# Kernel tuning notes

Measured on AMD Instinct MI355X. Metric: run time of the kernel, lower is better.

Reference implementation:

```python
import jax, jax.numpy as jnp
import numpy as np
from jax import lax

N_LAYERS = 4
D_MODEL = 256
D_INNER = 512   # expand * d_model
D_STATE = 16
D_CONV = 4
DT_RANK = 16    # ceil(d_model/16)
N_FEATURES = 32
N_CLASSES = 3
BATCH, SEQ = 8, 2048


def _layernorm(x, w, b, eps=1e-5):
    mu = x.mean(-1, keepdims=True)
    var = ((x - mu) ** 2).mean(-1, keepdims=True)
    return (x - mu) * lax.rsqrt(var + eps) * w + b


def _silu(x):
    return x * jax.nn.sigmoid(x)


def _ssm(xc, xpW, dtW, dtB, A_log, D):
    # xc: (B,S,d_inner)
    xd = xc @ xpW                                    # (B,S,dt_rank+2*d_state)
    dt_r = xd[..., :DT_RANK]
    Bm = xd[..., DT_RANK:DT_RANK + D_STATE]          # (B,S,N)
    Cm = xd[..., DT_RANK + D_STATE:]                 # (B,S,N)
    dt = jax.nn.softplus(dt_r @ dtW + dtB)           # (B,S,d_inner)
    A = -jnp.exp(A_log)                              # (d_inner,N)
    dA = jnp.exp(dt[..., None] * A)                  # (B,S,d_inner,N)
    dBx = dt[..., None] * Bm[:, :, None, :] * xc[..., None]  # (B,S,d_inner,N)

    def step(h, inp):
        dA_t, dBx_t, C_t = inp                       # (B,d_inner,N),(B,d_inner,N),(B,N)
        h = dA_t * h + dBx_t
        y_t = (h * C_t[:, None, :]).sum(-1)          # (B,d_inner)
        return h, y_t

    h0 = jnp.zeros((xc.shape[0], D_INNER, D_STATE), xc.dtype)
    xs = (dA.transpose(1, 0, 2, 3), dBx.transpose(1, 0, 2, 3), Cm.transpose(1, 0, 2))
    _, ys = lax.scan(step, h0, xs)                   # (S,B,d_inner)
    y = ys.transpose(1, 0, 2)
    return y + xc * D


def _mamba_block(x, inW, convW, convB, xpW, dtW, dtB, A_log, D, outW):
    xz = x @ inW                                     # (B,S,2*d_inner)
    xs, z = xz[..., :D_INNER], xz[..., D_INNER:]
    # causal depthwise conv1d (left-pad d_conv-1)
    xp = jnp.pad(xs, ((0, 0), (D_CONV - 1, 0), (0, 0)))
    xc = lax.conv_general_dilated(
        xp, convW, window_strides=(1,), padding='VALID',
        dimension_numbers=('NWC', 'WIO', 'NWC'),
        feature_group_count=D_INNER) + convB
    xc = _silu(xc)
    y = _ssm(xc, xpW, dtW, dtB, A_log, D)
    y = y * _silu(z)
    return y @ outW


def setup_inputs() -> dict:
    key = jax.random.key(0)
    ks = jax.random.split(key, 20)
    s = 0.02
    L = N_LAYERS
    inp = {
        'x': jax.random.normal(ks[0], (BATCH, SEQ, N_FEATURES), jnp.float32),
        'in_w': jax.random.normal(ks[1], (N_FEATURES, D_MODEL), jnp.float32) * s,
        'in_b': jnp.zeros((D_MODEL,), jnp.float32),
        'ln_w': jnp.ones((L, D_MODEL), jnp.float32),
        'ln_b': jnp.zeros((L, D_MODEL), jnp.float32),
        'inW': jax.random.normal(ks[2], (L, D_MODEL, 2 * D_INNER), jnp.float32) * s,
        'convW': jax.random.normal(ks[3], (L, D_CONV, 1, D_INNER), jnp.float32) * s,
        'convB': jnp.zeros((L, D_INNER), jnp.float32),
        'xpW': jax.random.normal(ks[4], (L, D_INNER, DT_RANK + 2 * D_STATE), jnp.float32) * s,
        'dtW': jax.random.uniform(ks[5], (L, DT_RANK, D_INNER), jnp.float32,
                                  -DT_RANK ** -0.5, DT_RANK ** -0.5),
        'A_log': jnp.broadcast_to(jnp.log(jnp.arange(1, D_STATE + 1, dtype=jnp.float32)),
                                  (L, D_INNER, D_STATE)).copy(),
        'D': jnp.ones((L, D_INNER), jnp.float32),
        'outW': jax.random.normal(ks[6], (L, D_INNER, D_MODEL), jnp.float32) * s,
        'fln_w': jnp.ones((D_MODEL,), jnp.float32),
        'fln_b': jnp.zeros((D_MODEL,), jnp.float32),
        'h1W': jax.random.normal(ks[7], (D_MODEL, D_MODEL // 2), jnp.float32) * s,
        'h1b': jnp.zeros((D_MODEL // 2,), jnp.float32),
        'h2W': jax.random.normal(ks[8], (D_MODEL // 2, N_CLASSES), jnp.float32) * s,
        'h2b': jnp.zeros((N_CLASSES,), jnp.float32),
    }
    # dt bias init: inv softplus of dt ~ LogUniform(dt_min, dt_max)
    dt_min, dt_max = 1e-3, 0.1
    u = jax.random.uniform(ks[9], (L, D_INNER), jnp.float32)
    dt = jnp.clip(jnp.exp(u * (np.log(dt_max) - np.log(dt_min)) + np.log(dt_min)), 1e-4)
    inp['dtB'] = dt + jnp.log(-jnp.expm1(-dt))
    return inp


def reference(x, in_w, in_b, ln_w, ln_b, inW, convW, convB, xpW, dtW, dtB,
              A_log, D, outW, fln_w, fln_b, h1W, h1b, h2W, h2b):
    h = x @ in_w + in_b                              # (B,S,d_model); dropout is eval-mode identity
    for i in range(N_LAYERS):
        h = h + _mamba_block(_layernorm(h, ln_w[i], ln_b[i]),
                             inW[i], convW[i], convB[i], xpW[i],
                             dtW[i], dtB[i], A_log[i], D[i], outW[i])
    h = _layernorm(h, fln_w, fln_b)
    last = h[:, -1]                                  # (B,d_model)
    hidden = jax.nn.gelu(last @ h1W + h1b)
    return hidden @ h2W + h2b                        # (B,n_classes)
```

## Files before the change

### kernel.cpp

```cpp
#include <hip/hip_runtime.h>
#include <math.h>

namespace {

constexpr int NL = 4;
constexpr int DM = 256;
constexpr int DI = 512;
constexpr int DS = 16;
constexpr int DR = 16;
constexpr int NF = 32;
constexpr int NB = 8;
constexpr int T  = 2048;
constexpr int ROWS = NB * T;
constexpr int XD = DR + 2 * DS;
constexpr int NC = 64;
constexpr int CL = T / NC;
constexpr int SCN = NB * DI * DS;

constexpr float LOG2E = 1.44269504088896341f;
constexpr float LN2   = 0.69314718055994531f;

typedef __attribute__((ext_vector_type(4))) float f32x4;
typedef __attribute__((ext_vector_type(8))) short bf16x8;
typedef __attribute__((ext_vector_type(4))) short s16x4;

__device__ __forceinline__ float fexp2(float x) { return __builtin_amdgcn_exp2f(x); }
__device__ __forceinline__ float frcp(float x)  { return __builtin_amdgcn_rcpf(x); }
__device__ __forceinline__ float flog2(float x) { return __builtin_amdgcn_logf(x); }

__device__ __forceinline__ float siluf(float x) {
    return x * frcp(1.f + fexp2(-LOG2E * x));
}
__device__ __forceinline__ float softplusf(float x) {
    return fmaxf(x, 0.f) + LN2 * flog2(1.f + fexp2(-LOG2E * fabsf(x)));
}
__device__ __forceinline__ short f2bf(float f) {
    union { float f; unsigned u; } c; c.f = f;
    unsigned r = (c.u + 0x7FFFu + ((c.u >> 16) & 1u)) >> 16;
    return (short)r;
}
__device__ __forceinline__ float bf2f(short s) {
    union { unsigned u; float f; } c; c.u = ((unsigned)(unsigned short)s) << 16;
    return c.f;
}
__device__ __forceinline__ void powers16(float g, float* a) {
    float g2 = g * g, g4 = g2 * g2, g8 = g4 * g4;
    a[0] = g;        a[1] = g2;       a[2] = g * g2;   a[3] = g4;
    a[4] = g * g4;   a[5] = g2 * g4;  a[6] = a[2] * g4; a[7] = g8;
    a[8] = g * g8;   a[9] = g2 * g8;  a[10] = a[2] * g8; a[11] = g4 * g8;
    a[12] = a[4] * g8; a[13] = a[5] * g8; a[14] = a[6] * g8; a[15] = g8 * g8;
}

__global__ void wtrans(const float* __restrict__ src, short* __restrict__ dst,
                       int K, int N, int Npad, int perL_dst)
{
    const int idx = blockIdx.x * 256 + threadIdx.x;
    const int l = idx / perL_dst;
    const int r = idx - l * perL_dst;
    const unsigned n = (unsigned)r / (unsigned)K;
    const unsigned k = (unsigned)r - n * (unsigned)K;
    float v = (n < (unsigned)N) ? src[(size_t)l * K * N + k * N + n] : 0.f;
    dst[idx] = f2bf(v);
}

__global__ void prep_dtWt(const float* __restrict__ dtW, float* __restrict__ dtWt)
{
    const int idx = blockIdx.x * 256 + threadIdx.x;
    const int l = idx / (DI * DR);
    const int r0 = idx - l * (DI * DR);
    const int d = r0 / DR, rr = r0 - d * DR;
    dtWt[idx] = dtW[(size_t)l * DR * DI + rr * DI + d];
}

__global__ void prep_A2(const float* __restrict__ A_log, float* __restrict__ negA2)
{
    const int i = blockIdx.x * 256 + threadIdx.x;
    negA2[i] = -LOG2E * fexp2(LOG2E * A_log[i]);
}

__global__ void cvt_bf16(const float* __restrict__ src, short* __restrict__ dst)
{
    const int i = blockIdx.x * 256 + threadIdx.x;
    dst[i] = f2bf(src[i]);
}

template <int EP>
__global__ void gemm_mfma(const short* __restrict__ A, const short* __restrict__ Bt,
                          float* __restrict__ C, short* __restrict__ Cs0,
                          short* __restrict__ Cs1, const float* __restrict__ bias,
                          int K, int lda, int ldc, int Ncut, int NXB, int NYB)
{
    __shared__ short smem[7680];
    const int bid = blockIdx.x;
    const int xcd = bid & 7, j = bid >> 3;
    const int by = xcd * (NYB >> 3) + j / NXB;
    const int bx = j - (j / NXB) * NXB;
    const int m0 = by * 128;
    const int n0 = bx * 64;

    const int tid = threadIdx.x;
    const int lane = tid & 63, w = tid >> 6;
    const int wr = w >> 1, wc = w & 1;
    const int lr = lane & 15, lk = lane >> 4;

    f32x4 acc[4][2] = {};
    for (int k0 = 0; k0 < K; k0 += 32) {
        __syncthreads();
#pragma unroll
        for (int i = 0; i < 2; ++i) {
            int c = tid + i * 256;
            int row = c >> 2, seg = c & 3;
            bf16x8 v = *(const bf16x8*)(A + (size_t)(m0 + row) * lda + k0 + seg * 8);
            *(bf16x8*)(&smem[row * 40 + seg * 8]) = v;
        }
        {
            int row = tid >> 2, seg = tid & 3;
            bf16x8 v = *(const bf16x8*)(Bt + (size_t)(n0 + row) * K + k0 + seg * 8);
            *(bf16x8*)(&smem[5120 + row * 40 + seg * 8]) = v;
        }
        __syncthreads();
        bf16x8 af[4], bfr[2];
#pragma unroll
        for (int m = 0; m < 4; ++m)
            af[m] = *(const bf16x8*)(&smem[(wr * 64 + m * 16 + lr) * 40 + lk * 8]);
#pragma unroll
        for (int n = 0; n < 2; ++n)
            bfr[n] = *(const bf16x8*)(&smem[5120 + (wc * 32 + n * 16 + lr) * 40 + lk * 8]);
#pragma unroll
        for (int m = 0; m < 4; ++m)
#pragma unroll
            for (int n = 0; n < 2; ++n)
                acc[m][n] = __builtin_amdgcn_mfma_f32_16x16x32_bf16(af[m], bfr[n], acc[m][n], 0, 0, 0);
    }
#pragma unroll
    for (int m = 0; m < 4; ++m) {
#pragma unroll
        for (int n = 0; n < 2; ++n) {
            const int col = n0 + wc * 32 + n * 16 + lr;
#pragma unroll
            for (int j2 = 0; j2 < 4; ++j2) {
                const int row = m0 + wr * 64 + m * 16 + lk * 4 + j2;
                const float v = acc[m][n][j2];
                if (EP == 0) {
                    if (col < DI) Cs0[(size_t)row * DI + col] = f2bf(v);
                    else          Cs1[(size_t)row * DI + col - DI] = f2bf(siluf(v));
                } else if (EP == 1) {
                    if (col < Ncut) C[(size_t)row * ldc + col] = v;
                } else if (EP == 2) {
                    C[(size_t)row * ldc + col] += v;
                } else {
                    C[(size_t)row * ldc + col] = v + bias[col];
                }
            }
        }
    }
}

__global__ void layernorm_kernel(const float* __restrict__ x,
                                 const float* __restrict__ w,
                                 const float* __restrict__ b,
                                 short* __restrict__ out)
{
    const int row = blockIdx.x;
    const int t = threadIdx.x;
    const int wid = t >> 6, lane = t & 63;
    __shared__ float red[4];

    float v = x[row * DM + t];
    float s = v;
#pragma unroll
    for (int o = 32; o >= 1; o >>= 1) s += __shfl_xor(s, o);
    if (lane == 0) red[wid] = s;
    __syncthreads();
    float mu = (red[0] + red[1] + red[2] + red[3]) * (1.f / DM);
    __syncthreads();

    float d = v - mu;
    float q = d * d;
#pragma unroll
    for (int o = 32; o >= 1; o >>= 1) q += __shfl_xor(q, o);
    if (lane == 0) red[wid] = q;
    __syncthreads();
    float var = (red[0] + red[1] + red[2] + red[3]) * (1.f / DM);

    out[row * DM + t] = f2bf(d * (1.f / sqrtf(var + 1e-5f)) * w[t] + b[t]);
}

__global__ void conv_silu_kernel(const short* __restrict__ xsb,
                                 const float* __restrict__ W,
                                 const float* __restrict__ Bc,
                                 short* __restrict__ xcb)
{
    const int idx = blockIdx.x * 256 + threadIdx.x;
    const int c4 = idx & (DI / 4 - 1);
    const int bt = idx >> 7;
    const int t = bt & (T - 1);
    const int c = c4 * 4;
    f32x4 acc = *(const f32x4*)(Bc + c);
#pragma unroll
    for (int k = 0; k < 4; ++k) {
        int tt = t + k - 3;
        if (tt >= 0) {
            s16x4 v = *(const s16x4*)(xsb + (size_t)(bt + k - 3) * DI + c);
            f32x4 wv = *(const f32x4*)(W + k * DI + c);
#pragma unroll
            for (int q = 0; q < 4; ++q) acc[q] += bf2f(v[q]) * wv[q];
        }
    }
    s16x4 o;
#pragma unroll
    for (int q = 0; q < 4; ++q) o[q] = f2bf(siluf(acc[q]));
    *(s16x4*)(xcb + (size_t)idx * 4) = o;
}

__global__ void scan_pass1(const float* __restrict__ xd,
                           const short* __restrict__ xcb,
                           const float* __restrict__ negA2,
                           const float* __restrict__ dtWt,
                           const float* __restrict__ dtB,
                           float* __restrict__ P, float* __restrict__ S)
{
    __shared__ float lds[CL][32];
    const int d = blockIdx.x * 256 + threadIdx.x;
    const int c = blockIdx.y;
    const int b = blockIdx.z;
    const int row0 = b * T + c * CL;

    {
        int t = threadIdx.x >> 3, seg = threadIdx.x & 7;
        *(f32x4*)&lds[t][seg * 4] =
            *(const f32x4*)(xd + (size_t)(row0 + t) * XD + seg * 4);
    }
    float A2[DS], h[DS], wcol[DR];
#pragma unroll
    for (int q = 0; q < 4; ++q) {
        *(f32x4*)&A2[q * 4]   = *(const f32x4*)(negA2 + d * DS + q * 4);
        *(f32x4*)&wcol[q * 4] = *(const f32x4*)(dtWt + d * DR + q * 4);
    }
    bool fastb = true;
#pragma unroll
    for (int s = 1; s < DS; ++s)
        fastb = fastb && (fabsf(A2[s] - A2[0] * (float)(s + 1)) <= 1e-4f * fabsf(A2[s]));
    const bool fast = __all(fastb);
#pragma unroll
    for (int s = 0; s < DS; ++s) h[s] = 0.f;
    const float dtBd = dtB[d];
    float sdt = 0.f;
    __syncthreads();

    for (int t = 0; t < CL; ++t) {
        float xcv = bf2f(xcb[(size_t)(row0 + t) * DI + d]);
        float accd = dtBd;
#pragma unroll
        for (int q = 0; q < 4; ++q) {
            f32x4 xr = *(const f32x4*)&lds[t][q * 4];
            accd += xr[0] * wcol[q * 4] + xr[1] * wcol[q * 4 + 1]
                  + xr[2] * wcol[q * 4 + 2] + xr[3] * wcol[q * 4 + 3];
        }
        float dtv = softplusf(accd);
        float dx = dtv * xcv;
        sdt += dtv;
        float a[DS];
        if (fast) powers16(fexp2(dtv * A2[0]), a);
        else {
#pragma unroll
            for (int s = 0; s < DS; ++s) a[s] = fexp2(dtv * A2[s]);
        }
#pragma unroll
        for (int q = 0; q < 4; ++q) {
            f32x4 Bv = *(const f32x4*)&lds[t][16 + q * 4];
#pragma unroll
            for (int s = 0; s < 4; ++s)
                h[q * 4 + s] = a[q * 4 + s] * h[q * 4 + s] + dx * Bv[s];
        }
    }
    float pa[DS];
    if (fast) powers16(fexp2(A2[0] * sdt), pa);
    else {
#pragma unroll
        for (int s = 0; s < DS; ++s) pa[s] = fexp2(A2[s] * sdt);
    }
    const size_t base = (size_t)c * SCN + ((size_t)b * DI + d) * DS;
#pragma unroll
    for (int q = 0; q < 4; ++q) {
        *(f32x4*)(S + base + q * 4) = *(f32x4*)&h[q * 4];
        *(f32x4*)(P + base + q * 4) = *(f32x4*)&pa[q * 4];
    }
}

__global__ void scan_combine(float* __restrict__ P, const float* __restrict__ S)
{
    const int idx3 = blockIdx.x * blockDim.x + threadIdx.x;
    float h = 0.f;
    for (int c = 0; c < NC; ++c) {
        float pc = P[c * SCN + idx3];
        float sc = S[c * SCN + idx3];
        P[c * SCN + idx3] = h;
        h = pc * h + sc;
    }
}

__global__ void scan_pass2(const float* __restrict__ xd,
                           const short* __restrict__ xcb,
                           const float* __restrict__ negA2,
                           const float* __restrict__ dtWt,
                           const float* __restrict__ dtB,
                           const float* __restrict__ Dv,
                           const float* __restrict__ H,
                           const short* __restrict__ zgb,
                           short* __restrict__ yb)
{
    __shared__ float lds[CL][48];
    const int d = blockIdx.x * 256 + threadIdx.x;
    const int c = blockIdx.y;
    const int b = blockIdx.z;
    const int row0 = b * T + c * CL;

    for (int c0 = threadIdx.x; c0 < CL * 12; c0 += 256) {
        int t = c0 / 12, seg = c0 - t * 12;
        *(f32x4*)&lds[t][seg * 4] =
            *(const f32x4*)(xd + (size_t)(row0 + t) * XD + seg * 4);
    }
    float A2[DS], h[DS], wcol[DR];
#pragma unroll
    for (int q = 0; q < 4; ++q) {
        *(f32x4*)&A2[q * 4]   = *(const f32x4*)(negA2 + d * DS + q * 4);
        *(f32x4*)&wcol[q * 4] = *(const f32x4*)(dtWt + d * DR + q * 4);
    }
    bool fastb = true;
#pragma unroll
    for (int s = 1; s < DS; ++s)
        fastb = fastb && (fabsf(A2[s] - A2[0] * (float)(s + 1)) <= 1e-4f * fabsf(A2[s]));
    const bool fast = __all(fastb);
    const size_t base = (size_t)c * SCN + ((size_t)b * DI + d) * DS;
#pragma unroll
    for (int q = 0; q < 4; ++q)
        *(f32x4*)&h[q * 4] = *(const f32x4*)(H + base + q * 4);
    const float dtBd = dtB[d];
    const float Dd = Dv[d];
    __syncthreads();

    for (int t = 0; t < CL; ++t) {
        const size_t row = (size_t)(row0 + t);
        float xcv = bf2f(xcb[row * DI + d]);
        float zg  = bf2f(zgb[row * DI + d]);
        float accd = dtBd;
#pragma unroll
        for (int q = 0; q < 4; ++q) {
            f32x4 xr = *(const f32x4*)&lds[t][q * 4];
            accd += xr[0] * wcol[q * 4] + xr[1] * wcol[q * 4 + 1]
                  + xr[2] * wcol[q * 4 + 2] + xr[3] * wcol[q * 4 + 3];
        }
        float dtv = softplusf(accd);
        float dx = dtv * xcv;
        float a[DS];
        if (fast) powers16(fexp2(dtv * A2[0]), a);
        else {
#pragma unroll
            for (int s = 0; s < DS; ++s) a[s] = fexp2(dtv * A2[s]);
        }
        float acc0 = 0.f, acc1 = 0.f, acc2 = 0.f, acc3 = 0.f;
#pragma unroll
        for (int q = 0; q < 4; ++q) {
            f32x4 Bv = *(const f32x4*)&lds[t][16 + q * 4];
            f32x4 Cv = *(const f32x4*)&lds[t][32 + q * 4];
            h[q * 4 + 0] = a[q * 4 + 0] * h[q * 4 + 0] + dx * Bv[0];
            acc0 += h[q * 4 + 0] * Cv[0];
            h[q * 4 + 1] = a[q * 4 + 1] * h[q * 4 + 1] + dx * Bv[1];
            acc1 += h[q * 4 + 1] * Cv[1];
            h[q * 4 + 2] = a[q * 4 + 2] * h[q * 4 + 2] + dx * Bv[2];
            acc2 += h[q * 4 + 2] * Cv[2];
            h[q * 4 + 3] = a[q * 4 + 3] * h[q * 4 + 3] + dx * Bv[3];
            acc3 += h[q * 4 + 3] * Cv[3];
        }
        float yv = (acc0 + acc1) + (acc2 + acc3);
        yb[row * DI + d] = f2bf((yv + xcv * Dd) * zg);
    }
}

__global__ void head_kernel(const float* __restrict__ h,
                            const float* __restrict__ fw, const float* __restrict__ fb,
                            const float* __restrict__ h1W, const float* __restrict__ h1b,
                            const float* __restrict__ h2W, const float* __restrict__ h2b,
                            float* __restrict__ out)
{
    const int bi = blockIdx.x;
    const int t = threadIdx.x;
    const int wid = t >> 6, lane = t & 63;
    __shared__ float red[4];
    __shared__ float ln[DM];
    __shared__ float hid[DM / 2];

    const float* row = h + ((bi + 1) * T - 1) * DM;
    float v = row[t];
    float s = v;
#pragma unroll
    for (int o = 32; o >= 1; o >>= 1) s += __shfl_xor(s, o);
    if (lane == 0) red[wid] = s;
    __syncthreads();
    float mu = (red[0] + red[1] + red[2] + red[3]) * (1.f / DM);
    __syncthreads();
    float d = v - mu;
    float q = d * d;
#pragma unroll
    for (int o = 32; o >= 1; o >>= 1) q += __shfl_xor(q, o);
    if (lane == 0) red[wid] = q;
    __syncthreads();
    float var = (red[0] + red[1] + red[2] + red[3]) * (1.f / DM);
    ln[t] = d * (1.f / sqrtf(var + 1e-5f)) * fw[t] + fb[t];
    __syncthreads();

    if (t < DM / 2) {
        float acc = h1b[t];
        for (int k = 0; k < DM; ++k) acc += ln[k] * h1W[k * (DM / 2) + t];
        float x3 = acc * acc * acc;
        hid[t] = 0.5f * acc * (1.f + tanhf(0.7978845608028654f * (acc + 0.044715f * x3)));
    }
    __syncthreads();
    if (t < 3) {
        float acc = h2b[t];
        for (int k = 0; k < DM / 2; ++k) acc += hid[k] * h2W[k * 3 + t];
        out[bi * 3 + t] = acc;
    }
}

}

extern "C" void kernel_launch(void* const* d_in, const int* in_sizes, int n_in,
                              void* d_out, int out_size, void* d_ws, size_t ws_size,
                              hipStream_t stream)
{
    (void)in_sizes; (void)n_in; (void)out_size; (void)ws_size;
    const float* x     = (const float*)d_in[0];
    const float* in_w  = (const float*)d_in[1];
    const float* in_b  = (const float*)d_in[2];
    const float* ln_w  = (const float*)d_in[3];
    const float* ln_b  = (const float*)d_in[4];
    const float* inW   = (const float*)d_in[5];
    const float* convW = (const float*)d_in[6];
    const float* convB = (const float*)d_in[7];
    const float* xpW   = (const float*)d_in[8];
    const float* dtW   = (const float*)d_in[9];
    const float* A_log = (const float*)d_in[10];
    const float* Dv    = (const float*)d_in[11];
    const float* outW  = (const float*)d_in[12];
    const float* fln_w = (const float*)d_in[13];
    const float* fln_b = (const float*)d_in[14];
    const float* h1W   = (const float*)d_in[15];
    const float* h1b   = (const float*)d_in[16];
    const float* h2W   = (const float*)d_in[17];
    const float* h2b   = (const float*)d_in[18];
    const float* dtB   = (const float*)d_in[19];
    float* out = (float*)d_out;

    float* w = (float*)d_ws;
    float* hbuf  = w;  w += ROWS * DM;
    float* xd    = w;  w += ROWS * XD;
    float* P     = w;  w += (size_t)SCN * NC;
    float* S     = w;  w += (size_t)SCN * NC;
    float* negA2 = w;  w += NL * DI * DS;
    float* dtWt  = w;  w += NL * DI * DR;
    short* xlnb  = (short*)w;
    short* xb    = xlnb + (size_t)ROWS * DM;
    short* xsb   = xb   + (size_t)ROWS * NF;
    short* zgb   = xsb  + (size_t)ROWS * DI;
    short* xcb   = zgb  + (size_t)ROWS * DI;
    short* yb    = xcb  + (size_t)ROWS * DI;
    short* inWt  = yb   + (size_t)ROWS * DI;
    short* xpWt  = inWt + (size_t)NL * 1024 * DM;
    short* outWt = xpWt + (size_t)NL * 64 * DI;
    short* inwT  = outWt + (size_t)NL * DM * DI;

    wtrans<<<NL * 1024 * DM / 256, 256, 0, stream>>>(inW, inWt, DM, 1024, 1024, 1024 * DM);
    wtrans<<<NL * 64 * DI / 256, 256, 0, stream>>>(xpW, xpWt, DI, XD, 64, 64 * DI);
    wtrans<<<NL * DM * DI / 256, 256, 0, stream>>>(outW, outWt, DI, DM, DM, DM * DI);
    wtrans<<<DM * NF / 256, 256, 0, stream>>>(in_w, inwT, NF, DM, DM, DM * NF);
    prep_dtWt<<<NL * DI * DR / 256, 256, 0, stream>>>(dtW, dtWt);
    prep_A2<<<NL * DI * DS / 256, 256, 0, stream>>>(A_log, negA2);
    cvt_bf16<<<ROWS * NF / 256, 256, 0, stream>>>(x, xb);

    gemm_mfma<3><<<(DM / 64) * (ROWS / 128), 256, 0, stream>>>(
        xb, inwT, hbuf, nullptr, nullptr, in_b, NF, NF, DM, 0, DM / 64, ROWS / 128);

    for (int i = 0; i < NL; ++i) {
        layernorm_kernel<<<ROWS, DM, 0, stream>>>(hbuf, ln_w + i * DM, ln_b + i * DM, xlnb);

        gemm_mfma<0><<<(1024 / 64) * (ROWS / 128), 256, 0, stream>>>(
            xlnb, inWt + (size_t)i * 1024 * DM, nullptr, xsb, zgb, nullptr,
            DM, DM, 0, 0, 1024 / 64, ROWS / 128);

        conv_silu_kernel<<<ROWS * DI / 1024, 256, 0, stream>>>(
            xsb, convW + i * 4 * DI, convB + i * DI, xcb);

        gemm_mfma<1><<<1 * (ROWS / 128), 256, 0, stream>>>(
            xcb, xpWt + (size_t)i * 64 * DI, xd, nullptr, nullptr, nullptr,
            DI, DI, XD, XD, 1, ROWS / 128);

        scan_pass1<<<dim3(DI / 256, NC, NB), 256, 0, stream>>>(
            xd, xcb, negA2 + i * DI * DS, dtWt + i * DI * DR, dtB + i * DI, P, S);
        scan_combine<<<SCN / 256, 256, 0, stream>>>(P, S);
        scan_pass2<<<dim3(DI / 256, NC, NB), 256, 0, stream>>>(
            xd, xcb, negA2 + i * DI * DS, dtWt + i * DI * DR, dtB + i * DI,
            Dv + i * DI, P, zgb, yb);

        gemm_mfma<2><<<(DM / 64) * (ROWS / 128), 256, 0, stream>>>(
            yb, outWt + (size_t)i * DM * DI, hbuf, nullptr, nullptr, nullptr,
            DI, DI, DM, 0, DM / 64, ROWS / 128);
    }

    head_kernel<<<NB, DM, 0, stream>>>(hbuf, fln_w, fln_b, h1W, h1b, h2W, h2b, out);
}
```

Baseline: 644.5 us.

## Fuse chunked scan passes into one cooperative kernel with grid syncs

Replaces the three scan kernels (pass1, combine, pass2) with one cooperative kernel that uses grid-wide syncs between phases. Chunk decay products are recomputed from stored per-chunk dt sums instead of writing a P array, and the carried states are written back in place into S. The x-projection GEMM also gets a 64-row tile variant so it launches more blocks. The aim is to cut launch overhead and P traffic. In exchange it needs all 1024 blocks co-resident under launch_bounds(256,4), and grid.sync adds its own cost.

```diff
diff --git a/kernel.cpp b/kernel.cpp
--- a/kernel.cpp
+++ b/kernel.cpp
@@ -1,4 +1,5 @@
 #include <hip/hip_runtime.h>
+#include <hip/hip_cooperative_groups.h>
 #include <math.h>
 
 namespace {
@@ -84,18 +85,19 @@
     dst[i] = f2bf(src[i]);
 }
 
-template <int EP>
+template <int EP, int BM>
 __global__ void gemm_mfma(const short* __restrict__ A, const short* __restrict__ Bt,
                           float* __restrict__ C, short* __restrict__ Cs0,
                           short* __restrict__ Cs1, const float* __restrict__ bias,
                           int K, int lda, int ldc, int Ncut, int NXB, int NYB)
 {
-    __shared__ short smem[7680];
+    constexpr int MF = BM / 32;
+    __shared__ short smem[BM * 40 + 64 * 40];
     const int bid = blockIdx.x;
     const int xcd = bid & 7, j = bid >> 3;
     const int by = xcd * (NYB >> 3) + j / NXB;
     const int bx = j - (j / NXB) * NXB;
-    const int m0 = by * 128;
+    const int m0 = by * BM;
     const int n0 = bx * 64;
 
     const int tid = threadIdx.x;
@@ -103,11 +105,11 @@
     const int wr = w >> 1, wc = w & 1;
     const int lr = lane & 15, lk = lane >> 4;
 
-    f32x4 acc[4][2] = {};
+    f32x4 acc[MF][2] = {};
     for (int k0 = 0; k0 < K; k0 += 32) {
         __syncthreads();
 #pragma unroll
-        for (int i = 0; i < 2; ++i) {
+        for (int i = 0; i < BM / 64; ++i) {
             int c = tid + i * 256;
             int row = c >> 2, seg = c & 3;
             bf16x8 v = *(const bf16x8*)(A + (size_t)(m0 + row) * lda + k0 + seg * 8);
@@ -116,30 +118,30 @@
         {
             int row = tid >> 2, seg = tid & 3;
             bf16x8 v = *(const bf16x8*)(Bt + (size_t)(n0 + row) * K + k0 + seg * 8);
-            *(bf16x8*)(&smem[5120 + row * 40 + seg * 8]) = v;
+            *(bf16x8*)(&smem[BM * 40 + row * 40 + seg * 8]) = v;
         }
         __syncthreads();
-        bf16x8 af[4], bfr[2];
-#pragma unroll
-        for (int m = 0; m < 4; ++m)
-            af[m] = *(const bf16x8*)(&smem[(wr * 64 + m * 16 + lr) * 40 + lk * 8]);
+        bf16x8 af[MF], bfr[2];
+#pragma unroll
+        for (int m = 0; m < MF; ++m)
+            af[m] = *(const bf16x8*)(&smem[(wr * (BM / 2) + m * 16 + lr) * 40 + lk * 8]);
 #pragma unroll
         for (int n = 0; n < 2; ++n)
-            bfr[n] = *(const bf16x8*)(&smem[5120 + (wc * 32 + n * 16 + lr) * 40 + lk * 8]);
-#pragma unroll
-        for (int m = 0; m < 4; ++m)
+            bfr[n] = *(const bf16x8*)(&smem[BM * 40 + (wc * 32 + n * 16 + lr) * 40 + lk * 8]);
+#pragma unroll
+        for (int m = 0; m < MF; ++m)
 #pragma unroll
             for (int n = 0; n < 2; ++n)
                 acc[m][n] = __builtin_amdgcn_mfma_f32_16x16x32_bf16(af[m], bfr[n], acc[m][n], 0, 0, 0);
     }
 #pragma unroll
-    for (int m = 0; m < 4; ++m) {
+    for (int m = 0; m < MF; ++m) {
 #pragma unroll
         for (int n = 0; n < 2; ++n) {
             const int col = n0 + wc * 32 + n * 16 + lr;
 #pragma unroll
             for (int j2 = 0; j2 < 4; ++j2) {
-                const int row = m0 + wr * 64 + m * 16 + lk * 4 + j2;
+                const int row = m0 + wr * (BM / 2) + m * 16 + lk * 4 + j2;
                 const float v = acc[m][n][j2];
                 if (EP == 0) {
                     if (col < DI) Cs0[(size_t)row * DI + col] = f2bf(v);
@@ -213,21 +215,24 @@
     *(s16x4*)(xcb + (size_t)idx * 4) = o;
 }
 
-__global__ void scan_pass1(const float* __restrict__ xd,
-                           const short* __restrict__ xcb,
-                           const float* __restrict__ negA2,
-                           const float* __restrict__ dtWt,
-                           const float* __restrict__ dtB,
-                           float* __restrict__ P, float* __restrict__ S)
-{
-    __shared__ float lds[CL][32];
-    const int d = blockIdx.x * 256 + threadIdx.x;
-    const int c = blockIdx.y;
-    const int b = blockIdx.z;
+__global__ __launch_bounds__(256, 4) void scan_fused(
+    const float* __restrict__ xd, const short* __restrict__ xcb,
+    const float* __restrict__ negA2, const float* __restrict__ dtWt,
+    const float* __restrict__ dtB, const float* __restrict__ Dv,
+    const short* __restrict__ zgb, float* __restrict__ S,
+    float* __restrict__ sdtb, short* __restrict__ yb)
+{
+    cooperative_groups::grid_group grid = cooperative_groups::this_grid();
+    __shared__ float lds[CL][48];
+    const int flat = blockIdx.x;
+    const int db = flat & (DI / 256 - 1);
+    const int c  = (flat >> 1) & (NC - 1);
+    const int b  = flat >> 7;
+    const int d  = db * 256 + threadIdx.x;
     const int row0 = b * T + c * CL;
 
-    {
-        int t = threadIdx.x >> 3, seg = threadIdx.x & 7;
+    for (int c0 = threadIdx.x; c0 < CL * 12; c0 += 256) {
+        int t = c0 / 12, seg = c0 - t * 12;
         *(f32x4*)&lds[t][seg * 4] =
             *(const f32x4*)(xd + (size_t)(row0 + t) * XD + seg * 4);
     }
@@ -242,9 +247,9 @@
     for (int s = 1; s < DS; ++s)
         fastb = fastb && (fabsf(A2[s] - A2[0] * (float)(s + 1)) <= 1e-4f * fabsf(A2[s]));
     const bool fast = __all(fastb);
+    const float dtBd = dtB[d];
 #pragma unroll
     for (int s = 0; s < DS; ++s) h[s] = 0.f;
-    const float dtBd = dtB[d];
     float sdt = 0.f;
     __syncthreads();
 
@@ -274,71 +279,33 @@
                 h[q * 4 + s] = a[q * 4 + s] * h[q * 4 + s] + dx * Bv[s];
         }
     }
-    float pa[DS];
-    if (fast) powers16(fexp2(A2[0] * sdt), pa);
-    else {
-#pragma unroll
-        for (int s = 0; s < DS; ++s) pa[s] = fexp2(A2[s] * sdt);
-    }
     const size_t base = (size_t)c * SCN + ((size_t)b * DI + d) * DS;
 #pragma unroll
-    for (int q = 0; q < 4; ++q) {
+    for (int q = 0; q < 4; ++q)
         *(f32x4*)(S + base + q * 4) = *(f32x4*)&h[q * 4];
-        *(f32x4*)(P + base + q * 4) = *(f32x4*)&pa[q * 4];
-    }
-}
-
-__global__ void scan_combine(float* __restrict__ P, const float* __restrict__ S)
-{
-    const int idx3 = blockIdx.x * blockDim.x + threadIdx.x;
-    float h = 0.f;
-    for (int c = 0; c < NC; ++c) {
-        float pc = P[c * SCN + idx3];
-        float sc = S[c * SCN + idx3];
-        P[c * SCN + idx3] = h;
-        h = pc * h + sc;
-    }
-}
-
-__global__ void scan_pass2(const float* __restrict__ xd,
-                           const short* __restrict__ xcb,
-                           const float* __restrict__ negA2,
-                           const float* __restrict__ dtWt,
-                           const float* __restrict__ dtB,
-                           const float* __restrict__ Dv,
-                           const float* __restrict__ H,
-                           const short* __restrict__ zgb,
-                           short* __restrict__ yb)
-{
-    __shared__ float lds[CL][48];
-    const int d = blockIdx.x * 256 + threadIdx.x;
-    const int c = blockIdx.y;
-    const int b = blockIdx.z;
-    const int row0 = b * T + c * CL;
-
-    for (int c0 = threadIdx.x; c0 < CL * 12; c0 += 256) {
-        int t = c0 / 12, seg = c0 - t * 12;
-        *(f32x4*)&lds[t][seg * 4] =
-            *(const f32x4*)(xd + (size_t)(row0 + t) * XD + seg * 4);
-    }
-    float A2[DS], h[DS], wcol[DR];
-#pragma unroll
-    for (int q = 0; q < 4; ++q) {
-        *(f32x4*)&A2[q * 4]   = *(const f32x4*)(negA2 + d * DS + q * 4);
-        *(f32x4*)&wcol[q * 4] = *(const f32x4*)(dtWt + d * DR + q * 4);
-    }
-    bool fastb = true;
-#pragma unroll
-    for (int s = 1; s < DS; ++s)
-        fastb = fastb && (fabsf(A2[s] - A2[0] * (float)(s + 1)) <= 1e-4f * fabsf(A2[s]));
-    const bool fast = __all(fastb);
-    const size_t base = (size_t)c * SCN + ((size_t)b * DI + d) * DS;
+    sdtb[c * (NB * DI) + b * DI + d] = sdt;
+
+    grid.sync();
+
+    if (flat < SCN / 256) {
+        const int idx3 = flat * 256 + threadIdx.x;
+        const int bd = idx3 >> 4;
+        const float A2c = negA2[(bd & (DI - 1)) * DS + (idx3 & 15)];
+        float hh = 0.f;
+        for (int cc = 0; cc < NC; ++cc) {
+            float sc = S[(size_t)cc * SCN + idx3];
+            float pc = fexp2(A2c * sdtb[cc * (NB * DI) + bd]);
+            S[(size_t)cc * SCN + idx3] = hh;
+            hh = pc * hh + sc;
+        }
+    }
+
+    grid.sync();
+
 #pragma unroll
     for (int q = 0; q < 4; ++q)
-        *(f32x4*)&h[q * 4] = *(const f32x4*)(H + base + q * 4);
-    const float dtBd = dtB[d];
+        *(f32x4*)&h[q * 4] = *(const f32x4*)(S + base + q * 4);
     const float Dd = Dv[d];
-    __syncthreads();
 
     for (int t = 0; t < CL; ++t) {
         const size_t row = (size_t)(row0 + t);
@@ -456,8 +423,8 @@
     float* w = (float*)d_ws;
     float* hbuf  = w;  w += ROWS * DM;
     float* xd    = w;  w += ROWS * XD;
-    float* P     = w;  w += (size_t)SCN * NC;
     float* S     = w;  w += (size_t)SCN * NC;
+    float* sdtb  = w;  w += NC * NB * DI;
     float* negA2 = w;  w += NL * DI * DS;
     float* dtWt  = w;  w += NL * DI * DR;
     short* xlnb  = (short*)w;
@@ -479,31 +446,42 @@
     prep_A2<<<NL * DI * DS / 256, 256, 0, stream>>>(A_log, negA2);
     cvt_bf16<<<ROWS * NF / 256, 256, 0, stream>>>(x, xb);
 
-    gemm_mfma<3><<<(DM / 64) * (ROWS / 128), 256, 0, stream>>>(
+    gemm_mfma<3, 128><<<(DM / 64) * (ROWS / 128), 256, 0, stream>>>(
         xb, inwT, hbuf, nullptr, nullptr, in_b, NF, NF, DM, 0, DM / 64, ROWS / 128);
 
     for (int i = 0; i < NL; ++i) {
         layernorm_kernel<<<ROWS, DM, 0, stream>>>(hbuf, ln_w + i * DM, ln_b + i * DM, xlnb);
 
-        gemm_mfma<0><<<(1024 / 64) * (ROWS / 128), 256, 0, stream>>>(
+        gemm_mfma<0, 128><<<(1024 / 64) * (ROWS / 128), 256, 0, stream>>>(
             xlnb, inWt + (size_t)i * 1024 * DM, nullptr, xsb, zgb, nullptr,
             DM, DM, 0, 0, 1024 / 64, ROWS / 128);
 
         conv_silu_kernel<<<ROWS * DI / 1024, 256, 0, stream>>>(
             xsb, convW + i * 4 * DI, convB + i * DI, xcb);
 
-        gemm_mfma<1><<<1 * (ROWS / 128), 256, 0, stream>>>(
+        gemm_mfma<1, 64><<<1 * (ROWS / 64), 256, 0, stream>>>(
             xcb, xpWt + (size_t)i * 64 * DI, xd, nullptr, nullptr, nullptr,
-            DI, DI, XD, XD, 1, ROWS / 128);
-
-        scan_pass1<<<dim3(DI / 256, NC, NB), 256, 0, stream>>>(
-            xd, xcb, negA2 + i * DI * DS, dtWt + i * DI * DR, dtB + i * DI, P, S);
-        scan_combine<<<SCN / 256, 256, 0, stream>>>(P, S);
-        scan_pass2<<<dim3(DI / 256, NC, NB), 256, 0, stream>>>(
-            xd, xcb, negA2 + i * DI * DS, dtWt + i * DI * DR, dtB + i * DI,
-            Dv + i * DI, P, zgb, yb);
-
-        gemm_mfma<2><<<(DM / 64) * (ROWS / 128), 256, 0, stream>>>(
+            DI, DI, XD, XD, 1, ROWS / 64);
+
+        {
+            const float* xd_p    = xd;
+            const short* xcb_p   = xcb;
+            const float* negA2_p = negA2 + i * DI * DS;
+            const float* dtWt_p  = dtWt + i * DI * DR;
+            const float* dtB_p   = dtB + i * DI;
+            const float* Dv_p    = Dv + i * DI;
+            const short* zgb_p   = zgb;
+            float* S_p    = S;
+            float* sdtb_p = sdtb;
+            short* yb_p   = yb;
+            void* args[] = {&xd_p, &xcb_p, &negA2_p, &dtWt_p, &dtB_p,
+                            &Dv_p, &zgb_p, &S_p, &sdtb_p, &yb_p};
+            hipLaunchCooperativeKernel((const void*)scan_fused,
+                                       dim3(NB * NC * (DI / 256)), dim3(256),
+                                       args, 0, stream);
+        }
+
+        gemm_mfma<2, 128><<<(DM / 64) * (ROWS / 128), 256, 0, stream>>>(
             yb, outWt + (size_t)i * DM * DI, hbuf, nullptr, nullptr, nullptr,
             DI, DI, DM, 0, DM / 64, ROWS / 128);
     }
```

Result: slower. 1.689 ms (+162.0%).

## Drop chunk-decay buffer P and recompute decay from per-chunk dt sums; smaller xproj tile

Applied to the files above, without the earlier changes.

Scan pass1 now writes only the chunk end state S and a per-(chunk,batch,channel) sum of dt, instead of also writing a full decay array P the size of S. scan_combine recomputes the chunk decay as exp2(A2*sdt) and stores the prefix state into S in place, which pass2 then reads. This roughly halves the scan's intermediate global traffic at the cost of one exp2 per element in combine. Separately, the GEMM is templated on block-M, and the narrow x_proj GEMM uses 64-row tiles so it launches twice as many blocks.

```diff
diff --git a/kernel.cpp b/kernel.cpp
--- a/kernel.cpp
+++ b/kernel.cpp
@@ -84,18 +84,19 @@
     dst[i] = f2bf(src[i]);
 }
 
-template <int EP>
+template <int EP, int BM>
 __global__ void gemm_mfma(const short* __restrict__ A, const short* __restrict__ Bt,
                           float* __restrict__ C, short* __restrict__ Cs0,
                           short* __restrict__ Cs1, const float* __restrict__ bias,
                           int K, int lda, int ldc, int Ncut, int NXB, int NYB)
 {
-    __shared__ short smem[7680];
+    constexpr int MF = BM / 32;
+    __shared__ short smem[BM * 40 + 64 * 40];
     const int bid = blockIdx.x;
     const int xcd = bid & 7, j = bid >> 3;
     const int by = xcd * (NYB >> 3) + j / NXB;
     const int bx = j - (j / NXB) * NXB;
-    const int m0 = by * 128;
+    const int m0 = by * BM;
     const int n0 = bx * 64;
 
     const int tid = threadIdx.x;
@@ -103,11 +104,11 @@
     const int wr = w >> 1, wc = w & 1;
     const int lr = lane & 15, lk = lane >> 4;
 
-    f32x4 acc[4][2] = {};
+    f32x4 acc[MF][2] = {};
     for (int k0 = 0; k0 < K; k0 += 32) {
         __syncthreads();
 #pragma unroll
-        for (int i = 0; i < 2; ++i) {
+        for (int i = 0; i < BM / 64; ++i) {
             int c = tid + i * 256;
             int row = c >> 2, seg = c & 3;
             bf16x8 v = *(const bf16x8*)(A + (size_t)(m0 + row) * lda + k0 + seg * 8);
@@ -116,30 +117,30 @@
         {
             int row = tid >> 2, seg = tid & 3;
             bf16x8 v = *(const bf16x8*)(Bt + (size_t)(n0 + row) * K + k0 + seg * 8);
-            *(bf16x8*)(&smem[5120 + row * 40 + seg * 8]) = v;
+            *(bf16x8*)(&smem[BM * 40 + row * 40 + seg * 8]) = v;
         }
         __syncthreads();
-        bf16x8 af[4], bfr[2];
-#pragma unroll
-        for (int m = 0; m < 4; ++m)
-            af[m] = *(const bf16x8*)(&smem[(wr * 64 + m * 16 + lr) * 40 + lk * 8]);
+        bf16x8 af[MF], bfr[2];
+#pragma unroll
+        for (int m = 0; m < MF; ++m)
+            af[m] = *(const bf16x8*)(&smem[(wr * (BM / 2) + m * 16 + lr) * 40 + lk * 8]);
 #pragma unroll
         for (int n = 0; n < 2; ++n)
-            bfr[n] = *(const bf16x8*)(&smem[5120 + (wc * 32 + n * 16 + lr) * 40 + lk * 8]);
-#pragma unroll
-        for (int m = 0; m < 4; ++m)
+            bfr[n] = *(const bf16x8*)(&smem[BM * 40 + (wc * 32 + n * 16 + lr) * 40 + lk * 8]);
+#pragma unroll
+        for (int m = 0; m < MF; ++m)
 #pragma unroll
             for (int n = 0; n < 2; ++n)
                 acc[m][n] = __builtin_amdgcn_mfma_f32_16x16x32_bf16(af[m], bfr[n], acc[m][n], 0, 0, 0);
     }
 #pragma unroll
-    for (int m = 0; m < 4; ++m) {
+    for (int m = 0; m < MF; ++m) {
 #pragma unroll
         for (int n = 0; n < 2; ++n) {
             const int col = n0 + wc * 32 + n * 16 + lr;
 #pragma unroll
             for (int j2 = 0; j2 < 4; ++j2) {
-                const int row = m0 + wr * 64 + m * 16 + lk * 4 + j2;
+                const int row = m0 + wr * (BM / 2) + m * 16 + lk * 4 + j2;
                 const float v = acc[m][n][j2];
                 if (EP == 0) {
                     if (col < DI) Cs0[(size_t)row * DI + col] = f2bf(v);
@@ -218,7 +219,7 @@
                            const float* __restrict__ negA2,
                            const float* __restrict__ dtWt,
                            const float* __restrict__ dtB,
-                           float* __restrict__ P, float* __restrict__ S)
+                           float* __restrict__ S, float* __restrict__ sdtb)
 {
     __shared__ float lds[CL][32];
     const int d = blockIdx.x * 256 + threadIdx.x;
@@ -274,28 +275,24 @@
                 h[q * 4 + s] = a[q * 4 + s] * h[q * 4 + s] + dx * Bv[s];
         }
     }
-    float pa[DS];
-    if (fast) powers16(fexp2(A2[0] * sdt), pa);
-    else {
-#pragma unroll
-        for (int s = 0; s < DS; ++s) pa[s] = fexp2(A2[s] * sdt);
-    }
     const size_t base = (size_t)c * SCN + ((size_t)b * DI + d) * DS;
 #pragma unroll
-    for (int q = 0; q < 4; ++q) {
+    for (int q = 0; q < 4; ++q)
         *(f32x4*)(S + base + q * 4) = *(f32x4*)&h[q * 4];
-        *(f32x4*)(P + base + q * 4) = *(f32x4*)&pa[q * 4];
-    }
-}
-
-__global__ void scan_combine(float* __restrict__ P, const float* __restrict__ S)
+    sdtb[c * (NB * DI) + b * DI + d] = sdt;
+}
+
+__global__ void scan_combine(float* __restrict__ S, const float* __restrict__ sdtb,
+                             const float* __restrict__ negA2)
 {
     const int idx3 = blockIdx.x * blockDim.x + threadIdx.x;
+    const int bd = idx3 >> 4;
+    const float A2c = negA2[(bd & (DI - 1)) * DS + (idx3 & 15)];
     float h = 0.f;
     for (int c = 0; c < NC; ++c) {
-        float pc = P[c * SCN + idx3];
-        float sc = S[c * SCN + idx3];
-        P[c * SCN + idx3] = h;
+        float sc = S[(size_t)c * SCN + idx3];
+        float pc = fexp2(A2c * sdtb[c * (NB * DI) + bd]);
+        S[(size_t)c * SCN + idx3] = h;
         h = pc * h + sc;
     }
 }
@@ -456,8 +453,8 @@
     float* w = (float*)d_ws;
     float* hbuf  = w;  w += ROWS * DM;
     float* xd    = w;  w += ROWS * XD;
-    float* P     = w;  w += (size_t)SCN * NC;
     float* S     = w;  w += (size_t)SCN * NC;
+    float* sdtb  = w;  w += NC * NB * DI;
     float* negA2 = w;  w += NL * DI * DS;
     float* dtWt  = w;  w += NL * DI * DR;
     short* xlnb  = (short*)w;
@@ -479,31 +476,31 @@
     prep_A2<<<NL * DI * DS / 256, 256, 0, stream>>>(A_log, negA2);
     cvt_bf16<<<ROWS * NF / 256, 256, 0, stream>>>(x, xb);
 
-    gemm_mfma<3><<<(DM / 64) * (ROWS / 128), 256, 0, stream>>>(
+    gemm_mfma<3, 128><<<(DM / 64) * (ROWS / 128), 256, 0, stream>>>(
         xb, inwT, hbuf, nullptr, nullptr, in_b, NF, NF, DM, 0, DM / 64, ROWS / 128);
 
     for (int i = 0; i < NL; ++i) {
         layernorm_kernel<<<ROWS, DM, 0, stream>>>(hbuf, ln_w + i * DM, ln_b + i * DM, xlnb);
 
-        gemm_mfma<0><<<(1024 / 64) * (ROWS / 128), 256, 0, stream>>>(
+        gemm_mfma<0, 128><<<(1024 / 64) * (ROWS / 128), 256, 0, stream>>>(
             xlnb, inWt + (size_t)i * 1024 * DM, nullptr, xsb, zgb, nullptr,
             DM, DM, 0, 0, 1024 / 64, ROWS / 128);
 
         conv_silu_kernel<<<ROWS * DI / 1024, 256, 0, stream>>>(
             xsb, convW + i * 4 * DI, convB + i * DI, xcb);
 
-        gemm_mfma<1><<<1 * (ROWS / 128), 256, 0, stream>>>(
+        gemm_mfma<1, 64><<<1 * (ROWS / 64), 256, 0, stream>>>(
             xcb, xpWt + (size_t)i * 64 * DI, xd, nullptr, nullptr, nullptr,
-            DI, DI, XD, XD, 1, ROWS / 128);
+            DI, DI, XD, XD, 1, ROWS / 64);
 
         scan_pass1<<<dim3(DI / 256, NC, NB), 256, 0, stream>>>(
-            xd, xcb, negA2 + i * DI * DS, dtWt + i * DI * DR, dtB + i * DI, P, S);
-        scan_combine<<<SCN / 256, 256, 0, stream>>>(P, S);
+            xd, xcb, negA2 + i * DI * DS, dtWt + i * DI * DR, dtB + i * DI, S, sdtb);
+        scan_combine<<<SCN / 256, 256, 0, stream>>>(S, sdtb, negA2 + i * DI * DS);
         scan_pass2<<<dim3(DI / 256, NC, NB), 256, 0, stream>>>(
             xd, xcb, negA2 + i * DI * DS, dtWt + i * DI * DR, dtB + i * DI,
-            Dv + i * DI, P, zgb, yb);
-
-        gemm_mfma<2><<<(DM / 64) * (ROWS / 128), 256, 0, stream>>>(
+            Dv + i * DI, S, zgb, yb);
+
+        gemm_mfma<2, 128><<<(DM / 64) * (ROWS / 128), 256, 0, stream>>>(
             yb, outWt + (size_t)i * DM * DI, hbuf, nullptr, nullptr, nullptr,
             DI, DI, DM, 0, DM / 64, ROWS / 128);
     }
```

New measurement: 612.3 us. 1.05x faster.
